# Optimization experiments

Hardware: AMD Instinct MI355X
Metric: run time of the kernel (lower is better)

Reference implementation:

```python
import jax, jax.numpy as jnp
import numpy as np

EMB = 1024   # embedding_size = input_size // 2
HID = 1024   # hidden_size
B = 16384


def _glorot(key, shape):
    fan_in = shape[0]
    bound = 1.0 / np.sqrt(fan_in)
    return jax.random.uniform(key, shape, jnp.float32, -bound, bound)


def setup_inputs() -> dict:
    key = jax.random.key(0)
    ks = jax.random.split(key, 14)
    return {
        "inputs": jax.random.normal(ks[0], (B, 2 * EMB), jnp.float32),
        "state": jax.random.normal(ks[1], (B, HID), jnp.float32),
        # weights stored [in, out] (transpose of torch Linear layout)
        "Wr": _glorot(ks[2], (EMB + HID, HID)), "br": jnp.zeros((HID,), jnp.float32),
        "Wu": _glorot(ks[3], (EMB + HID, HID)), "bu": jnp.zeros((HID,), jnp.float32),
        "Wc": _glorot(ks[4], (EMB + HID, HID)), "bc": jnp.zeros((HID,), jnp.float32),
        "W1": _glorot(ks[5], (EMB, HID)), "b1": jnp.zeros((HID,), jnp.float32),
        "W2": _glorot(ks[6], (EMB, HID)), "b2": jnp.zeros((HID,), jnp.float32),
        "Wg": _glorot(ks[7], (2 * HID, HID)), "bg": jnp.zeros((HID,), jnp.float32),
    }


def reference(inputs, state, Wr, br, Wu, bu, Wc, bc, W1, b1, W2, b2, Wg, bg):
    # split input into semantic half and neighbor half
    x = inputs[:, :EMB]          # [B, EMB]
    neighbors = inputs[:, EMB:]  # [B, EMB]

    gate_inputs = jnp.concatenate([x, state], axis=1)            # [B, EMB+HID]
    r = jax.nn.sigmoid(gate_inputs @ Wr + br)                    # reset gate
    u = jax.nn.sigmoid(gate_inputs @ Wu + bu)                    # update gate
    c = jnp.tanh(jnp.concatenate([x, r * state], axis=1) @ Wc + bc)

    semantic_emb = jax.nn.relu(x @ W1 + b1)
    neighbor_emb = jax.nn.relu(neighbors @ W2 + b2)
    new_gate = jax.nn.sigmoid(
        jnp.concatenate([semantic_emb, neighbor_emb], axis=1) @ Wg + bg)

    new_h = u * state + (1.0 - u) * c * new_gate
    return new_h
```

## Files before the change

### kernel.cpp

```cpp
#include <hip/hip_runtime.h>
#include <hip/hip_bf16.h>
#include <math.h>

#define Bsz 16384
#define HIDc 1024

typedef __attribute__((ext_vector_type(8))) short short8_t;
typedef __attribute__((ext_vector_type(4))) float f32x4;
typedef __attribute__((ext_vector_type(4))) short s16x4;

typedef __attribute__((address_space(1))) const unsigned char* gp1_t;
typedef __attribute__((address_space(3))) unsigned char* lp3_t;

__device__ __forceinline__ float sigf(float x) { return 1.0f / (1.0f + __expf(-x)); }
__device__ __forceinline__ float tanh_fast(float x) {
  x = fminf(fmaxf(x, -10.f), 10.f);
  float t = __expf(2.f * x);
  return (t - 1.f) / (t + 1.f);
}

__device__ __forceinline__ int xcd_map(int bid, int nwg) {
  const int q = nwg >> 3, r = nwg & 7;
  const int xcd = bid & 7, idx = bid >> 3;
  return (xcd < r ? xcd * (q + 1) : r * (q + 1) + (xcd - r) * q) + idx;
}

__device__ __forceinline__ void stage64(const __hip_bfloat16* __restrict__ g, long ld,
                                        __hip_bfloat16* l, int wave, int lane) {
  const int rsub = lane >> 3;
  const int kx = ((lane & 7) ^ rsub) << 3;
#pragma unroll
  for (int i = 0; i < 4; ++i) {
    const int chunk = i * 4 + wave;
    const int row = chunk * 8 + rsub;
    const __hip_bfloat16* gp = g + (long)row * ld + kx;
    __hip_bfloat16* lp = l + chunk * 512 + lane * 8;
    __builtin_amdgcn_global_load_lds((gp1_t)gp, (lp3_t)lp, 16, 0, 0);
  }
}

__device__ __forceinline__ void gemm_acc(const __hip_bfloat16* __restrict__ A, long lda,
                                         const __hip_bfloat16* __restrict__ Wt, long ldw,
                                         int K,
                                         __hip_bfloat16* lA, __hip_bfloat16* lB,
                                         f32x4 acc[4][4]) {
  const int tid = threadIdx.x;
  const int wave = tid >> 6, lane = tid & 63;
  const int wr = wave >> 1, wc = wave & 1;
  const int lm = lane & 15, hi = lane >> 4, l7 = lane & 7;
  for (int k0 = 0; k0 < K; k0 += 64) {
    __syncthreads();
    stage64(A + k0, lda, lA, wave, lane);
    stage64(Wt + k0, ldw, lB, wave, lane);
    __syncthreads();
#pragma unroll
    for (int ks = 0; ks < 2; ++ks) {
      short8_t a8[4], b8[4];
      const int sl = ks * 4 + hi;
#pragma unroll
      for (int m = 0; m < 4; ++m) {
        const int r = wr * 64 + m * 16 + lm;
        a8[m] = *reinterpret_cast<const short8_t*>(lA + r * 64 + ((sl ^ l7) << 3));
      }
#pragma unroll
      for (int n = 0; n < 4; ++n) {
        const int r = wc * 64 + n * 16 + lm;
        b8[n] = *reinterpret_cast<const short8_t*>(lB + r * 64 + ((sl ^ l7) << 3));
      }
#pragma unroll
      for (int m = 0; m < 4; ++m)
#pragma unroll
        for (int n = 0; n < 4; ++n)
          acc[m][n] = __builtin_amdgcn_mfma_f32_16x16x32_bf16(a8[m], b8[n], acc[m][n], 0, 0, 0);
    }
  }
}

template <int EPI>
__global__ void gemm_k(const __hip_bfloat16* __restrict__ A, long lda,
                       const __hip_bfloat16* __restrict__ Wt, long ldw, int K, int nbx,
                       const float* __restrict__ bias0, const float* __restrict__ bias1,
                       const __hip_bfloat16* __restrict__ stbf,
                       const __hip_bfloat16* __restrict__ auxbf,
                       __hip_bfloat16* __restrict__ out0, __hip_bfloat16* __restrict__ out1) {
  __shared__ __hip_bfloat16 lA[128 * 64], lB[128 * 64];
  f32x4 acc[4][4];
#pragma unroll
  for (int m = 0; m < 4; ++m)
#pragma unroll
    for (int n = 0; n < 4; ++n) acc[m][n] = (f32x4){0.f, 0.f, 0.f, 0.f};

  const int wg = xcd_map(blockIdx.x, gridDim.x);
  const long mBase = (long)(wg / nbx) * 128;
  const long nBase = (long)(wg % nbx) * 128;
  gemm_acc(A + mBase * lda, lda, Wt + nBase * ldw, ldw, K, lA, lB, acc);

  const int tid = threadIdx.x, wave = tid >> 6, lane = tid & 63;
  const int wr = wave >> 1, wc = wave & 1, lm = lane & 15, hi = lane >> 4;
  const int row0 = (int)mBase + wr * 64 + hi * 4;
  const int col0 = (int)nBase + wc * 64 + lm;
#pragma unroll
  for (int m = 0; m < 4; ++m)
#pragma unroll
    for (int n = 0; n < 4; ++n)
#pragma unroll
      for (int j = 0; j < 4; ++j) {
        const long row = row0 + m * 16 + j;
        const int col = col0 + n * 16;
        const float v = acc[m][n][j];
        if (EPI == 0) {
          if (col < HIDc) {
            float rr = sigf(v + bias0[col]);
            float st = __bfloat162float(stbf[row * 2048 + 1024 + col]);
            out0[row * HIDc + col] = __float2bfloat16(rr * st);
          } else {
            int c = col - HIDc;
            out1[row * HIDc + c] = __float2bfloat16(sigf(v + bias1[c]));
          }
        } else if (EPI == 1) {
          if (col < HIDc) {
            out0[row * 2048 + col] = __float2bfloat16(fmaxf(v + bias0[col], 0.f));
          } else {
            int c = col - HIDc;
            out1[row * HIDc + c] = __float2bfloat16(v + bias1[c]);
          }
        } else if (EPI == 2) {
          out0[row * 2048 + HIDc + col] = __float2bfloat16(fmaxf(v + bias0[col], 0.f));
        } else {
          const long idx = row * HIDc + col;
          float cb = tanh_fast(v + __bfloat162float(auxbf[idx]));
          out0[idx] = __float2bfloat16(cb);
        }
      }
}

__global__ void final_g(const __hip_bfloat16* __restrict__ SN,
                        const __hip_bfloat16* __restrict__ Wgt,
                        const __hip_bfloat16* __restrict__ CB,
                        const __hip_bfloat16* __restrict__ U,
                        const __hip_bfloat16* __restrict__ stbf,
                        const float* __restrict__ bg,
                        float* __restrict__ out, int nbx) {
  __shared__ __hip_bfloat16 lA[128 * 64], lB[128 * 64];
  f32x4 acc[4][4];
#pragma unroll
  for (int m = 0; m < 4; ++m)
#pragma unroll
    for (int n = 0; n < 4; ++n) acc[m][n] = (f32x4){0.f, 0.f, 0.f, 0.f};

  const int wg = xcd_map(blockIdx.x, gridDim.x);
  const long mBase = (long)(wg / nbx) * 128;
  const long nBase = (long)(wg % nbx) * 128;
  gemm_acc(SN + mBase * 2048, 2048, Wgt + nBase * 2048, 2048, 2048, lA, lB, acc);

  const int tid = threadIdx.x, wave = tid >> 6, lane = tid & 63;
  const int wr = wave >> 1, wc = wave & 1, lm = lane & 15, hi = lane >> 4;
  const int row0 = (int)mBase + wr * 64 + hi * 4;
  const int col0 = (int)nBase + wc * 64 + lm;
#pragma unroll
  for (int m = 0; m < 4; ++m)
#pragma unroll
    for (int n = 0; n < 4; ++n)
#pragma unroll
      for (int j = 0; j < 4; ++j) {
        const long row = row0 + m * 16 + j;
        const int col = col0 + n * 16;
        const long idx = row * HIDc + col;
        float g = sigf(acc[m][n][j] + bg[col]);
        float u = __bfloat162float(U[idx]);
        float cb = __bfloat162float(CB[idx]);
        float st = __bfloat162float(stbf[row * 2048 + 1024 + col]);
        out[idx] = u * st + (1.f - u) * cb * g;
      }
}

__global__ void convert_k(const float4* __restrict__ in4, const float4* __restrict__ st4,
                          __hip_bfloat16* __restrict__ A1, __hip_bfloat16* __restrict__ NB) {
  const long NI4 = (long)Bsz * 2048 / 4;
  const long NS4 = (long)Bsz * 1024 / 4;
  for (long i = (long)blockIdx.x * blockDim.x + threadIdx.x; i < NI4 + NS4;
       i += (long)gridDim.x * blockDim.x) {
    float4 v;
    __hip_bfloat16* dst;
    if (i < NI4) {
      v = in4[i];
      long e = i << 2;
      long row = e >> 11;
      int col = (int)(e & 2047);
      dst = (col < 1024) ? (A1 + row * 2048 + col) : (NB + row * 1024 + (col - 1024));
    } else {
      long j = i - NI4;
      v = st4[j];
      long e = j << 2;
      long row = e >> 10;
      int col = (int)(e & 1023);
      dst = A1 + row * 2048 + 1024 + col;
    }
    union { __hip_bfloat16 h[4]; s16x4 s; } u;
    u.h[0] = __float2bfloat16(v.x);
    u.h[1] = __float2bfloat16(v.y);
    u.h[2] = __float2bfloat16(v.z);
    u.h[3] = __float2bfloat16(v.w);
    *reinterpret_cast<s16x4*>(dst) = u.s;
  }
}

__global__ void transpose_k(const float* __restrict__ in, int ldin,
                            __hip_bfloat16* __restrict__ out, long ldout) {
  __shared__ float t[32][33];
  const int k0 = blockIdx.x * 32, n0 = blockIdx.y * 32;
  const int tx = threadIdx.x, ty = threadIdx.y;
#pragma unroll
  for (int dy = 0; dy < 32; dy += 8)
    t[ty + dy][tx] = in[(long)(k0 + ty + dy) * ldin + n0 + tx];
  __syncthreads();
#pragma unroll
  for (int dy = 0; dy < 32; dy += 8)
    out[(long)(n0 + ty + dy) * ldout + k0 + tx] = __float2bfloat16(t[tx][ty + dy]);
}

extern "C" void kernel_launch(void* const* d_in, const int* in_sizes, int n_in,
                              void* d_out, int out_size, void* d_ws, size_t ws_size,
                              hipStream_t stream) {
  const float* inputs = (const float*)d_in[0];
  const float* state = (const float*)d_in[1];
  const float* Wr = (const float*)d_in[2];
  const float* br = (const float*)d_in[3];
  const float* Wu = (const float*)d_in[4];
  const float* bu = (const float*)d_in[5];
  const float* Wc = (const float*)d_in[6];
  const float* bc = (const float*)d_in[7];
  const float* W1 = (const float*)d_in[8];
  const float* b1 = (const float*)d_in[9];
  const float* W2 = (const float*)d_in[10];
  const float* b2 = (const float*)d_in[11];
  const float* Wg = (const float*)d_in[12];
  const float* bg = (const float*)d_in[13];
  float* out = (float*)d_out;

  char* ws = (char*)d_ws;
  __hip_bfloat16* A1    = (__hip_bfloat16*)(ws);
  __hip_bfloat16* NB    = (__hip_bfloat16*)(ws + 67108864L);
  __hip_bfloat16* RS    = (__hip_bfloat16*)(ws + 100663296L);
  __hip_bfloat16* Ub    = (__hip_bfloat16*)(ws + 134217728L);
  __hip_bfloat16* SN    = (__hip_bfloat16*)(ws + 167772160L);
  __hip_bfloat16* CXb   = (__hip_bfloat16*)(ws + 234881024L);
  __hip_bfloat16* Wru_t = (__hip_bfloat16*)(ws + 268435456L);
  __hip_bfloat16* W1cx_t= (__hip_bfloat16*)(ws + 276824064L);
  __hip_bfloat16* Wcb_t = (__hip_bfloat16*)(ws + 281018368L);
  __hip_bfloat16* W2_t  = (__hip_bfloat16*)(ws + 283115520L);
  __hip_bfloat16* Wg_t  = (__hip_bfloat16*)(ws + 285212672L);
  __hip_bfloat16* CB    = NB;

  convert_k<<<2048, 256, 0, stream>>>((const float4*)inputs, (const float4*)state, A1, NB);

  dim3 tb(32, 8);
  transpose_k<<<dim3(64, 32), tb, 0, stream>>>(Wr, 1024, Wru_t, 2048);
  transpose_k<<<dim3(64, 32), tb, 0, stream>>>(Wu, 1024, Wru_t + (long)1024 * 2048, 2048);
  transpose_k<<<dim3(32, 32), tb, 0, stream>>>(W1, 1024, W1cx_t, 1024);
  transpose_k<<<dim3(32, 32), tb, 0, stream>>>(Wc, 1024, W1cx_t + (long)1024 * 1024, 1024);
  transpose_k<<<dim3(32, 32), tb, 0, stream>>>(Wc + (long)1024 * 1024, 1024, Wcb_t, 1024);
  transpose_k<<<dim3(32, 32), tb, 0, stream>>>(W2, 1024, W2_t, 1024);
  transpose_k<<<dim3(64, 32), tb, 0, stream>>>(Wg, 1024, Wg_t, 2048);

  gemm_k<0><<<2048, 256, 0, stream>>>(A1, 2048, Wru_t, 2048, 2048, 16,
                                      br, bu, A1, nullptr, RS, Ub);
  gemm_k<1><<<2048, 256, 0, stream>>>(A1, 2048, W1cx_t, 1024, 1024, 16,
                                      b1, bc, nullptr, nullptr, SN, CXb);
  gemm_k<2><<<1024, 256, 0, stream>>>(NB, 1024, W2_t, 1024, 1024, 8,
                                      b2, nullptr, nullptr, nullptr, SN, nullptr);
  gemm_k<3><<<1024, 256, 0, stream>>>(RS, 1024, Wcb_t, 1024, 1024, 8,
                                      nullptr, nullptr, nullptr, CXb, CB, nullptr);
  final_g<<<1024, 256, 0, stream>>>(SN, Wg_t, CB, Ub, A1, bg, out, 8);
}
```

Measured before the change: 524.4 us.

## Replace 128x128 GEMMs with double-buffered 256x256 tiled 8-wave kernel

Replaces the single-buffered 128x128 tile GEMM kernels with a 256x256 tile, 512-thread kernel that double-buffers 64-wide K slices in 128 KB of LDS. It prefetches the next K slice with direct global-to-LDS loads while MFMAs run in four phases, using explicit barriers, setprio and waitcnt scheduling. The final gate GEMM is folded into the same template as a new epilogue. The aim is to overlap global loads with compute and raise data reuse per tile. In exchange it uses much more LDS and fewer, larger workgroups (256 to 512 blocks), which may lower occupancy and leave CUs unevenly loaded.

```diff
diff --git a/kernel.cpp b/kernel.cpp
--- a/kernel.cpp
+++ b/kernel.cpp
@@ -25,153 +25,170 @@
   return (xcd < r ? xcd * (q + 1) : r * (q + 1) + (xcd - r) * q) + idx;
 }
 
-__device__ __forceinline__ void stage64(const __hip_bfloat16* __restrict__ g, long ld,
-                                        __hip_bfloat16* l, int wave, int lane) {
-  const int rsub = lane >> 3;
-  const int kx = ((lane & 7) ^ rsub) << 3;
-#pragma unroll
-  for (int i = 0; i < 4; ++i) {
-    const int chunk = i * 4 + wave;
-    const int row = chunk * 8 + rsub;
-    const __hip_bfloat16* gp = g + (long)row * ld + kx;
-    __hip_bfloat16* lp = l + chunk * 512 + lane * 8;
-    __builtin_amdgcn_global_load_lds((gp1_t)gp, (lp3_t)lp, 16, 0, 0);
+__device__ __forceinline__ void stage_half(const __hip_bfloat16* __restrict__ g, long ld,
+                                           __hip_bfloat16* l, int tid) {
+#pragma unroll
+  for (int it = 0; it < 2; ++it) {
+    const int sid = it * 512 + tid;
+    const int row = sid >> 3, slot = sid & 7;
+    const int kx = (slot ^ (row & 7)) << 3;
+    __builtin_amdgcn_global_load_lds((gp1_t)(g + (long)row * ld + kx),
+                                     (lp3_t)(l + sid * 8), 16, 0, 0);
   }
 }
 
-__device__ __forceinline__ void gemm_acc(const __hip_bfloat16* __restrict__ A, long lda,
-                                         const __hip_bfloat16* __restrict__ Wt, long ldw,
-                                         int K,
-                                         __hip_bfloat16* lA, __hip_bfloat16* lB,
-                                         f32x4 acc[4][4]) {
+#define STAGE_TILE(dstbase, t) do {                                              \
+    stage_half(Ablk + (long)(t) * 64,             lda, (dstbase),         tid);  \
+    stage_half(Ablk + 128 * lda + (long)(t) * 64, lda, (dstbase) + 8192,  tid);  \
+    stage_half(Wblk + (long)(t) * 64,             ldw, (dstbase) + 16384, tid);  \
+    stage_half(Wblk + 128 * ldw + (long)(t) * 64, ldw, (dstbase) + 24576, tid);  \
+  } while (0)
+
+#define READ_A(AhB, qm)                                                          \
+  _Pragma("unroll") for (int m_ = 0; m_ < 4; ++m_)                               \
+    _Pragma("unroll") for (int k_ = 0; k_ < 2; ++k_)                             \
+      a8[m_][k_] = *reinterpret_cast<const short8_t*>(                           \
+          (AhB) + ((qm) * 64 + m_ * 16 + lm) * 64 + (((k_ * 4 + hi) ^ l7) << 3));
+
+#define READ_B(BhB, qn)                                                          \
+  _Pragma("unroll") for (int n_ = 0; n_ < 2; ++n_)                               \
+    _Pragma("unroll") for (int k_ = 0; k_ < 2; ++k_)                             \
+      b8[qn][n_][k_] = *reinterpret_cast<const short8_t*>(                       \
+          (BhB) + (wcl * 64 + (qn) * 32 + n_ * 16 + lm) * 64 + (((k_ * 4 + hi) ^ l7) << 3));
+
+#define PHASE(qm, qn, VM) do {                                                   \
+    __builtin_amdgcn_sched_barrier(0);                                           \
+    __builtin_amdgcn_s_barrier();                                                \
+    asm volatile("s_waitcnt lgkmcnt(0)" ::: "memory");                           \
+    __builtin_amdgcn_sched_barrier(0);                                           \
+    __builtin_amdgcn_s_setprio(1);                                               \
+    _Pragma("unroll") for (int m_ = 0; m_ < 4; ++m_)                             \
+      _Pragma("unroll") for (int n_ = 0; n_ < 2; ++n_)                           \
+        _Pragma("unroll") for (int k_ = 0; k_ < 2; ++k_)                         \
+          acc[qm][qn][m_][n_] = __builtin_amdgcn_mfma_f32_16x16x32_bf16(         \
+              a8[m_][k_], b8[qn][n_][k_], acc[qm][qn][m_][n_], 0, 0, 0);         \
+    __builtin_amdgcn_s_setprio(0);                                               \
+    __builtin_amdgcn_sched_barrier(0);                                           \
+    if (VM) {                                                                    \
+      asm volatile("s_waitcnt vmcnt(0)" ::: "memory");                           \
+      __builtin_amdgcn_sched_barrier(0);                                         \
+    }                                                                            \
+    __builtin_amdgcn_s_barrier();                                                \
+    __builtin_amdgcn_sched_barrier(0);                                           \
+  } while (0)
+
+template <int EPI>
+__global__ __launch_bounds__(512, 2)
+void gemm256(const __hip_bfloat16* __restrict__ A, long lda,
+             const __hip_bfloat16* __restrict__ Wt, long ldw, int K, int nbx,
+             const float* __restrict__ bias0, const float* __restrict__ bias1,
+             const __hip_bfloat16* __restrict__ stbf,
+             const __hip_bfloat16* __restrict__ auxbf,
+             const __hip_bfloat16* __restrict__ CB,
+             const __hip_bfloat16* __restrict__ U,
+             __hip_bfloat16* __restrict__ out0,
+             __hip_bfloat16* __restrict__ out1,
+             float* __restrict__ outf) {
+  __shared__ __hip_bfloat16 lds[65536];
   const int tid = threadIdx.x;
   const int wave = tid >> 6, lane = tid & 63;
-  const int wr = wave >> 1, wc = wave & 1;
+  const int wr = wave >> 2, wc = wave & 3, wcl = wc & 1;
   const int lm = lane & 15, hi = lane >> 4, l7 = lane & 7;
-  for (int k0 = 0; k0 < K; k0 += 64) {
-    __syncthreads();
-    stage64(A + k0, lda, lA, wave, lane);
-    stage64(Wt + k0, ldw, lB, wave, lane);
-    __syncthreads();
-#pragma unroll
-    for (int ks = 0; ks < 2; ++ks) {
-      short8_t a8[4], b8[4];
-      const int sl = ks * 4 + hi;
-#pragma unroll
-      for (int m = 0; m < 4; ++m) {
-        const int r = wr * 64 + m * 16 + lm;
-        a8[m] = *reinterpret_cast<const short8_t*>(lA + r * 64 + ((sl ^ l7) << 3));
-      }
-#pragma unroll
-      for (int n = 0; n < 4; ++n) {
-        const int r = wc * 64 + n * 16 + lm;
-        b8[n] = *reinterpret_cast<const short8_t*>(lB + r * 64 + ((sl ^ l7) << 3));
-      }
-#pragma unroll
-      for (int m = 0; m < 4; ++m)
-#pragma unroll
-        for (int n = 0; n < 4; ++n)
-          acc[m][n] = __builtin_amdgcn_mfma_f32_16x16x32_bf16(a8[m], b8[n], acc[m][n], 0, 0, 0);
+
+  const int wg = xcd_map(blockIdx.x, gridDim.x);
+  const long mBase = (long)(wg / nbx) * 256;
+  const long nBase = (long)(wg % nbx) * 256;
+  const __hip_bfloat16* Ablk = A + mBase * lda;
+  const __hip_bfloat16* Wblk = Wt + nBase * ldw;
+
+  f32x4 acc[2][2][4][2];
+#pragma unroll
+  for (int a = 0; a < 2; ++a)
+#pragma unroll
+    for (int b = 0; b < 2; ++b)
+#pragma unroll
+      for (int c = 0; c < 4; ++c)
+#pragma unroll
+        for (int d = 0; d < 2; ++d) acc[a][b][c][d] = (f32x4){0.f, 0.f, 0.f, 0.f};
+
+  short8_t a8[4][2], b8[2][2][2];
+
+  STAGE_TILE(lds, 0);
+  asm volatile("s_waitcnt vmcnt(0)" ::: "memory");
+  __builtin_amdgcn_s_barrier();
+  __builtin_amdgcn_sched_barrier(0);
+
+  const int NI = K >> 7;
+  for (int i = 0; i < NI; ++i) {
+    {
+      const __hip_bfloat16* AhB = lds + wr * 8192;
+      const __hip_bfloat16* BhB = lds + 16384 + (wc >> 1) * 8192;
+      READ_A(AhB, 0); READ_B(BhB, 0);
+      STAGE_TILE(lds + 32768, 2 * i + 1);
+      PHASE(0, 0, 0);
+      READ_B(BhB, 1);
+      PHASE(0, 1, 0);
+      READ_A(AhB, 1);
+      PHASE(1, 0, 0);
+      PHASE(1, 1, 1);
+    }
+    {
+      const __hip_bfloat16* AhB = lds + 32768 + wr * 8192;
+      const __hip_bfloat16* BhB = lds + 32768 + 16384 + (wc >> 1) * 8192;
+      READ_A(AhB, 0); READ_B(BhB, 0);
+      if (i + 1 < NI) STAGE_TILE(lds, 2 * i + 2);
+      PHASE(0, 0, 0);
+      READ_B(BhB, 1);
+      PHASE(0, 1, 0);
+      READ_A(AhB, 1);
+      PHASE(1, 0, 0);
+      PHASE(1, 1, 1);
     }
   }
-}
-
-template <int EPI>
-__global__ void gemm_k(const __hip_bfloat16* __restrict__ A, long lda,
-                       const __hip_bfloat16* __restrict__ Wt, long ldw, int K, int nbx,
-                       const float* __restrict__ bias0, const float* __restrict__ bias1,
-                       const __hip_bfloat16* __restrict__ stbf,
-                       const __hip_bfloat16* __restrict__ auxbf,
-                       __hip_bfloat16* __restrict__ out0, __hip_bfloat16* __restrict__ out1) {
-  __shared__ __hip_bfloat16 lA[128 * 64], lB[128 * 64];
-  f32x4 acc[4][4];
-#pragma unroll
-  for (int m = 0; m < 4; ++m)
-#pragma unroll
-    for (int n = 0; n < 4; ++n) acc[m][n] = (f32x4){0.f, 0.f, 0.f, 0.f};
-
-  const int wg = xcd_map(blockIdx.x, gridDim.x);
-  const long mBase = (long)(wg / nbx) * 128;
-  const long nBase = (long)(wg % nbx) * 128;
-  gemm_acc(A + mBase * lda, lda, Wt + nBase * ldw, ldw, K, lA, lB, acc);
-
-  const int tid = threadIdx.x, wave = tid >> 6, lane = tid & 63;
-  const int wr = wave >> 1, wc = wave & 1, lm = lane & 15, hi = lane >> 4;
-  const int row0 = (int)mBase + wr * 64 + hi * 4;
-  const int col0 = (int)nBase + wc * 64 + lm;
-#pragma unroll
-  for (int m = 0; m < 4; ++m)
-#pragma unroll
-    for (int n = 0; n < 4; ++n)
-#pragma unroll
-      for (int j = 0; j < 4; ++j) {
-        const long row = row0 + m * 16 + j;
-        const int col = col0 + n * 16;
-        const float v = acc[m][n][j];
-        if (EPI == 0) {
-          if (col < HIDc) {
-            float rr = sigf(v + bias0[col]);
-            float st = __bfloat162float(stbf[row * 2048 + 1024 + col]);
-            out0[row * HIDc + col] = __float2bfloat16(rr * st);
-          } else {
-            int c = col - HIDc;
-            out1[row * HIDc + c] = __float2bfloat16(sigf(v + bias1[c]));
+
+#pragma unroll
+  for (int qm = 0; qm < 2; ++qm)
+#pragma unroll
+    for (int qn = 0; qn < 2; ++qn)
+#pragma unroll
+      for (int m = 0; m < 4; ++m)
+#pragma unroll
+        for (int n = 0; n < 2; ++n)
+#pragma unroll
+          for (int j = 0; j < 4; ++j) {
+            const long row = mBase + wr * 128 + qm * 64 + m * 16 + hi * 4 + j;
+            const int col = (int)nBase + wc * 64 + qn * 32 + n * 16 + lm;
+            const float v = acc[qm][qn][m][n][j];
+            if (EPI == 0) {
+              if (col < HIDc) {
+                float rr = sigf(v + bias0[col]);
+                float st = __bfloat162float(stbf[row * 2048 + 1024 + col]);
+                out0[row * HIDc + col] = __float2bfloat16(rr * st);
+              } else {
+                int c = col - HIDc;
+                out1[row * HIDc + c] = __float2bfloat16(sigf(v + bias1[c]));
+              }
+            } else if (EPI == 1) {
+              if (col < HIDc) {
+                out0[row * 2048 + col] = __float2bfloat16(fmaxf(v + bias0[col], 0.f));
+              } else {
+                int c = col - HIDc;
+                out1[row * HIDc + c] = __float2bfloat16(v + bias1[c]);
+              }
+            } else if (EPI == 2) {
+              out0[row * 2048 + HIDc + col] = __float2bfloat16(fmaxf(v + bias0[col], 0.f));
+            } else if (EPI == 3) {
+              const long idx = row * HIDc + col;
+              out0[idx] = __float2bfloat16(tanh_fast(v + __bfloat162float(auxbf[idx])));
+            } else {
+              const long idx = row * HIDc + col;
+              float g = sigf(v + bias0[col]);
+              float u = __bfloat162float(U[idx]);
+              float cb = __bfloat162float(CB[idx]);
+              float st = __bfloat162float(stbf[row * 2048 + 1024 + col]);
+              outf[idx] = u * st + (1.f - u) * cb * g;
+            }
           }
-        } else if (EPI == 1) {
-          if (col < HIDc) {
-            out0[row * 2048 + col] = __float2bfloat16(fmaxf(v + bias0[col], 0.f));
-          } else {
-            int c = col - HIDc;
-            out1[row * HIDc + c] = __float2bfloat16(v + bias1[c]);
-          }
-        } else if (EPI == 2) {
-          out0[row * 2048 + HIDc + col] = __float2bfloat16(fmaxf(v + bias0[col], 0.f));
-        } else {
-          const long idx = row * HIDc + col;
-          float cb = tanh_fast(v + __bfloat162float(auxbf[idx]));
-          out0[idx] = __float2bfloat16(cb);
-        }
-      }
-}
-
-__global__ void final_g(const __hip_bfloat16* __restrict__ SN,
-                        const __hip_bfloat16* __restrict__ Wgt,
-                        const __hip_bfloat16* __restrict__ CB,
-                        const __hip_bfloat16* __restrict__ U,
-                        const __hip_bfloat16* __restrict__ stbf,
-                        const float* __restrict__ bg,
-                        float* __restrict__ out, int nbx) {
-  __shared__ __hip_bfloat16 lA[128 * 64], lB[128 * 64];
-  f32x4 acc[4][4];
-#pragma unroll
-  for (int m = 0; m < 4; ++m)
-#pragma unroll
-    for (int n = 0; n < 4; ++n) acc[m][n] = (f32x4){0.f, 0.f, 0.f, 0.f};
-
-  const int wg = xcd_map(blockIdx.x, gridDim.x);
-  const long mBase = (long)(wg / nbx) * 128;
-  const long nBase = (long)(wg % nbx) * 128;
-  gemm_acc(SN + mBase * 2048, 2048, Wgt + nBase * 2048, 2048, 2048, lA, lB, acc);
-
-  const int tid = threadIdx.x, wave = tid >> 6, lane = tid & 63;
-  const int wr = wave >> 1, wc = wave & 1, lm = lane & 15, hi = lane >> 4;
-  const int row0 = (int)mBase + wr * 64 + hi * 4;
-  const int col0 = (int)nBase + wc * 64 + lm;
-#pragma unroll
-  for (int m = 0; m < 4; ++m)
-#pragma unroll
-    for (int n = 0; n < 4; ++n)
-#pragma unroll
-      for (int j = 0; j < 4; ++j) {
-        const long row = row0 + m * 16 + j;
-        const int col = col0 + n * 16;
-        const long idx = row * HIDc + col;
-        float g = sigf(acc[m][n][j] + bg[col]);
-        float u = __bfloat162float(U[idx]);
-        float cb = __bfloat162float(CB[idx]);
-        float st = __bfloat162float(stbf[row * 2048 + 1024 + col]);
-        out[idx] = u * st + (1.f - u) * cb * g;
-      }
 }
 
 __global__ void convert_k(const float4* __restrict__ in4, const float4* __restrict__ st4,
@@ -263,13 +280,19 @@
   transpose_k<<<dim3(32, 32), tb, 0, stream>>>(W2, 1024, W2_t, 1024);
   transpose_k<<<dim3(64, 32), tb, 0, stream>>>(Wg, 1024, Wg_t, 2048);
 
-  gemm_k<0><<<2048, 256, 0, stream>>>(A1, 2048, Wru_t, 2048, 2048, 16,
-                                      br, bu, A1, nullptr, RS, Ub);
-  gemm_k<1><<<2048, 256, 0, stream>>>(A1, 2048, W1cx_t, 1024, 1024, 16,
-                                      b1, bc, nullptr, nullptr, SN, CXb);
-  gemm_k<2><<<1024, 256, 0, stream>>>(NB, 1024, W2_t, 1024, 1024, 8,
-                                      b2, nullptr, nullptr, nullptr, SN, nullptr);
-  gemm_k<3><<<1024, 256, 0, stream>>>(RS, 1024, Wcb_t, 1024, 1024, 8,
-                                      nullptr, nullptr, nullptr, CXb, CB, nullptr);
-  final_g<<<1024, 256, 0, stream>>>(SN, Wg_t, CB, Ub, A1, bg, out, 8);
-}
+  gemm256<0><<<512, 512, 0, stream>>>(A1, 2048, Wru_t, 2048, 2048, 8,
+                                      br, bu, A1, nullptr, nullptr, nullptr,
+                                      RS, Ub, nullptr);
+  gemm256<1><<<512, 512, 0, stream>>>(A1, 2048, W1cx_t, 1024, 1024, 8,
+                                      b1, bc, nullptr, nullptr, nullptr, nullptr,
+                                      SN, CXb, nullptr);
+  gemm256<2><<<256, 512, 0, stream>>>(NB, 1024, W2_t, 1024, 1024, 4,
+                                      b2, nullptr, nullptr, nullptr, nullptr, nullptr,
+                                      SN, nullptr, nullptr);
+  gemm256<3><<<256, 512, 0, stream>>>(RS, 1024, Wcb_t, 1024, 1024, 4,
+                                      nullptr, nullptr, nullptr, CXb, nullptr, nullptr,
+                                      CB, nullptr, nullptr);
+  gemm256<4><<<256, 512, 0, stream>>>(SN, 2048, Wg_t, 2048, 2048, 4,
+                                      bg, nullptr, A1, nullptr, CB, Ub,
+                                      nullptr, nullptr, out);
+}
```

New measurement: 584.1 us. 1.11x slower.
